# Kernel optimization log

Hardware: AMD Instinct MI355X
Metric: run time of the kernel (lower is better)

Reference implementation:

```python
import jax, jax.numpy as jnp
import numpy as np

B, T, D_IN = 128, 1024, 13
H = 256                      # total CfC units (hidden_units)
N_INTER, N_CMD, N_MOTOR = 77, 51, 128   # AutoNCP(256, 128) layer partition
SIZES = (N_INTER, N_CMD, N_MOTOR)
INS = (D_IN, N_INTER, N_CMD)


def setup_inputs() -> dict:
    key = jax.random.key(0)
    ks = iter(jax.random.split(key, 64))

    def w(shape):
        scale = 1.0 / np.sqrt(shape[-1])
        return jax.random.uniform(next(ks), shape, jnp.float32, -scale, scale)

    inp = {}
    inp["x"] = jax.random.normal(next(ks), (B, T, D_IN), dtype=jnp.float32)
    inp["lstm_Wih"] = w((4 * H, D_IN))
    inp["lstm_Whh"] = w((4 * H, H))
    inp["lstm_bih"] = w((4 * H,))
    inp["lstm_bhh"] = w((4 * H,))
    for l, (nin, nh) in enumerate(zip(INS, SIZES)):
        for nm in ("ff1", "ff2", "ta", "tb"):
            inp[f"l{l}_W{nm}"] = w((nh, nin + nh))
            inp[f"l{l}_b{nm}"] = w((nh,))
        # NCP input sparsity (~0.5 density) + all-ones recurrent block, as WiredCfCCell
        m_in = (jax.random.uniform(next(ks), (nh, nin)) < 0.5).astype(jnp.float32)
        inp[f"l{l}_mask"] = jnp.concatenate([m_in, jnp.ones((nh, nh), jnp.float32)], axis=1)
    inp["gyro_W"] = w((3, N_MOTOR)); inp["gyro_b"] = w((3,))
    inp["acc_W"] = w((3, N_MOTOR)); inp["acc_b"] = w((3,))
    inp["unc_W"] = w((6, N_MOTOR)); inp["unc_b"] = w((6,))
    return inp


def _cfc_cell(z, W1, b1, W2, b2, Wa, ba, Wb, bb, mask):
    # CfC cell, "default" mode, no backbone, ts = 1.0 (CfC called without timespans)
    ff1 = jnp.tanh(z @ (W1 * mask).T + b1)
    ff2 = jnp.tanh(z @ (W2 * mask).T + b2)
    t_interp = jax.nn.sigmoid(z @ Wa.T + ba + z @ Wb.T + bb)  # sigmoid(t_a*1 + t_b)
    return ff1 * (1.0 - t_interp) + t_interp * ff2


def _forward(x, lstm_Wih, lstm_Whh, lstm_bih, lstm_bhh, layer_params, masks,
             gyro_W, gyro_b, acc_W, acc_b, unc_W, unc_b):
    bsz = x.shape[0]
    h0 = jnp.zeros((bsz, H), x.dtype)
    c0 = jnp.zeros((bsz, H), x.dtype)
    b_lstm = lstm_bih + lstm_bhh

    def step(carry, x_t):
        h, c = carry
        # mixed-memory LSTM cell on the full state
        gates = x_t @ lstm_Wih.T + h @ lstm_Whh.T + b_lstm
        i, f, g, o = jnp.split(gates, 4, axis=-1)
        c = jax.nn.sigmoid(f) * c + jax.nn.sigmoid(i) * jnp.tanh(g)
        h = jax.nn.sigmoid(o) * jnp.tanh(c)
        # WiredCfCCell: sequential NCP layers (inter -> command -> motor)
        hs = (h[:, :N_INTER], h[:, N_INTER:N_INTER + N_CMD], h[:, N_INTER + N_CMD:])
        inp = x_t
        new_hs = []
        for l in range(3):
            inp = _cfc_cell(jnp.concatenate([inp, hs[l]], axis=-1), *layer_params[l], masks[l])
            new_hs.append(inp)
        h = jnp.concatenate(new_hs, axis=-1)
        return (h, c), new_hs[-1]

    _, motor = jax.lax.scan(step, (h0, c0), jnp.swapaxes(x, 0, 1))
    motor = jnp.swapaxes(motor, 0, 1)  # (B, T, N_MOTOR)
    pred = jnp.concatenate([motor @ gyro_W.T + gyro_b, motor @ acc_W.T + acc_b], axis=-1)
    uncertainty = jax.nn.softplus(motor @ unc_W.T + unc_b)
    return pred, uncertainty


def reference(x, lstm_Wih, lstm_Whh, lstm_bih, lstm_bhh,
              l0_Wff1, l0_bff1, l0_Wff2, l0_bff2, l0_Wta, l0_bta, l0_Wtb, l0_btb, l0_mask,
              l1_Wff1, l1_bff1, l1_Wff2, l1_bff2, l1_Wta, l1_bta, l1_Wtb, l1_btb, l1_mask,
              l2_Wff1, l2_bff1, l2_Wff2, l2_bff2, l2_Wta, l2_bta, l2_Wtb, l2_btb, l2_mask,
              gyro_W, gyro_b, acc_W, acc_b, unc_W, unc_b):
    layer_params = (
        (l0_Wff1, l0_bff1, l0_Wff2, l0_bff2, l0_Wta, l0_bta, l0_Wtb, l0_btb),
        (l1_Wff1, l1_bff1, l1_Wff2, l1_bff2, l1_Wta, l1_bta, l1_Wtb, l1_btb),
        (l2_Wff1, l2_bff1, l2_Wff2, l2_bff2, l2_Wta, l2_bta, l2_Wtb, l2_btb),
    )
    masks = (l0_mask, l1_mask, l2_mask)
    return _forward(x, lstm_Wih, lstm_Whh, lstm_bih, lstm_bhh, layer_params, masks,
                    gyro_W, gyro_b, acc_W, acc_b, unc_W, unc_b)
```

## Files before the change

kernel.cpp:

```cpp
#include <hip/hip_runtime.h>
#include <cstdint>

#define B_  128
#define T_  1024
#define DIN 13
#define HS  256
#define N0  77
#define N1  51
#define N2  128

#define QG   34
#define NRG  1024
#define Q0   12
#define NR0  308
#define Q1   16
#define NR1  204
#define Q2   23
#define NR2  512
#define Q2LDS 18

#define EXSTRIDE 256
#define X1O   0
#define X2O   128

typedef _Float16 h2_t __attribute__((ext_vector_type(2)));

static __device__ __forceinline__ uint32_t pk2(float a, float b) {
  h2_t v; v.x = (_Float16)a; v.y = (_Float16)b;
  return __builtin_bit_cast(uint32_t, v);
}
static __device__ __forceinline__ unsigned short f16b(float v) {
  return __builtin_bit_cast(unsigned short, (_Float16)v);
}
static __device__ __forceinline__ void st16(void* base, int idx, unsigned short v) {
  ((unsigned short*)base)[idx] = v;
}
static __device__ __forceinline__ float dot2f(uint32_t w, uint32_t z, float acc) {
#if __has_builtin(__builtin_amdgcn_fdot2)
  return __builtin_amdgcn_fdot2(__builtin_bit_cast(h2_t, w), __builtin_bit_cast(h2_t, z), acc, false);
#else
  h2_t a = __builtin_bit_cast(h2_t, w), b = __builtin_bit_cast(h2_t, z);
  return acc + (float)a.x * (float)b.x + (float)a.y * (float)b.y;
#endif
}
static __device__ __forceinline__ float dot8f(uint4 w, uint4 z, float acc) {
  acc = dot2f(w.x, z.x, acc);
  acc = dot2f(w.y, z.y, acc);
  acc = dot2f(w.z, z.z, acc);
  acc = dot2f(w.w, z.w, acc);
  return acc;
}
static __device__ __forceinline__ float sigf(float x) { return 1.f / (1.f + expf(-x)); }

static __device__ __forceinline__ void axpub(int* p, int tag, unsigned short v16) {
  __hip_atomic_store(p, (tag << 16) | (int)v16, __ATOMIC_RELAXED, __HIP_MEMORY_SCOPE_AGENT);
}
static __device__ __forceinline__ unsigned short axpoll(const int* p, int tag) {
  int w;
  do {
    w = __hip_atomic_load((int*)p, __ATOMIC_RELAXED, __HIP_MEMORY_SCOPE_AGENT);
  } while (((unsigned)w >> 16) != (unsigned)tag);
  return (unsigned short)(w & 0xFFFF);
}


__global__ void prep_gates3(const float* __restrict__ Wih, const float* __restrict__ Whh,
                            uint32_t* __restrict__ out) {
  int id = blockIdx.x * blockDim.x + threadIdx.x;
  if (id >= 136 * NRG) return;
  int k2 = id >> 10, row = id & (NRG - 1);
  float v[2];
#pragma unroll
  for (int j = 0; j < 2; ++j) {
    int e = 2 * k2 + j;
    float val = 0.f;
    if (e < 13) val = Wih[row * DIN + e];
    else if (e >= 16 && e < 144) val = Whh[row * HS + 128 + (e - 16)];
    else if (e >= 144 && e < 195) val = Whh[row * HS + 77 + (e - 144)];
    else if (e >= 195 && e < 272) val = Whh[row * HS + (e - 195)];
    v[j] = val;
  }
  out[((k2 >> 2) * NRG + row) * 4 + (k2 & 3)] = pk2(v[0], v[1]);
}

__global__ void prep_cfc2(const float* __restrict__ Wf1, const float* __restrict__ Wf2,
                          const float* __restrict__ Wta, const float* __restrict__ Wtb,
                          const float* __restrict__ mask,
                          int nh, int K, int NR, int K2,
                          int p0n, int p0c, int p1s, int p1n, int p1c,
                          uint32_t* __restrict__ out) {
  int id = blockIdx.x * blockDim.x + threadIdx.x;
  if (id >= NR * K2) return;
  int k2 = id / NR, r = id % NR;
  int mat = r / nh, o = r % nh;
  const float* W = (mat == 0) ? Wf1 : (mat == 1) ? Wf2 : (mat == 2) ? Wta : Wtb;
  float v[2];
#pragma unroll
  for (int j = 0; j < 2; ++j) {
    int e = 2 * k2 + j;
    int col = -1;
    if (e < p0n) col = p0c + e;
    else if (e >= p1s && e < p1s + p1n) col = p1c + (e - p1s);
    float val = 0.f;
    if (col >= 0) {
      val = W[o * K + col];
      if (mat < 2) val *= mask[o * K + col];
    }
    v[j] = val;
  }
  out[((k2 >> 2) * NR + r) * 4 + (k2 & 3)] = pk2(v[0], v[1]);
}


struct SMA {
  uint4 l0w[Q0 * NR0];
  uint4 l1w[Q1 * NR1];
  uint4 zb[2][QG];
  uint4 z0[Q0];
  uint4 z1[Q1];
  float garr[512];
  float ffb[NR0];
  float cb0[NR0];
  float cb1[NR1];
};
struct SMB {
  uint4 l2w[Q2LDS * NR2];
  uint4 zb[2][QG];
  uint4 z2[Q2];
  float garr[512];
  float ffb[NR2];
  float cb2[NR2];
  uint4 hwq[12][16];
  float hb[12];
};
static_assert(sizeof(SMA) <= 163840, "SMA too big");
static_assert(sizeof(SMB) <= 163840, "SMB too big");

struct PArgs {
  const float* x;
  const float* bih; const float* bhh;
  const float* b0[4]; const float* b1[4]; const float* b2[4];
  const float* gW; const float* gb; const float* aW; const float* ab;
  const float* uW; const float* ub;
  const uint4* wsG; const uint4* wsL0; const uint4* wsL1; const uint4* wsL2;
  int* ex;
  float* out;
};

__global__ __launch_bounds__(512, 2) void rnn_coop3(PArgs P) {
  extern __shared__ char smraw[];
  const int tid = threadIdx.x;
  const bool isA = (blockIdx.x < B_);
  const int b = blockIdx.x & (B_ - 1);
  int* EX = P.ex + b * EXSTRIDE;
  const float* xb = P.x + (size_t)b * T_ * DIN;
  const size_t UNC_OFF = (size_t)B_ * T_ * 6;

  if (isA) {
    SMA& sm = *(SMA*)smraw;
    for (int i = tid; i < Q0 * NR0; i += 512) sm.l0w[i] = P.wsL0[i];
    for (int i = tid; i < Q1 * NR1; i += 512) sm.l1w[i] = P.wsL1[i];
    for (int i = tid; i < NR0; i += 512) sm.cb0[i] = P.b0[i / N0][i % N0];
    for (int i = tid; i < NR1; i += 512) sm.cb1[i] = P.b1[i / N1][i % N1];
    {
      uint32_t* zz = (uint32_t*)sm.zb;
      for (int i = tid; i < (2 * QG + Q0 + Q1) * 4; i += 512) zz[i] = 0u;
    }
    const int grow = ((tid >> 7) << 8) | (tid & 127);
    const float bg = P.bih[grow] + P.bhh[grow];
    float c_r = 0.f;
    __syncthreads();
    if (tid < 13) st16(sm.zb[0], tid, f16b(xb[tid]));
    __syncthreads();
    uint4* zbc = sm.zb[0];
    uint4* zbn = sm.zb[1];
    {
      float acc = bg;
      acc = dot8f(P.wsG[0 * NRG + grow], zbc[0], acc);
      acc = dot8f(P.wsG[1 * NRG + grow], zbc[1], acc);
      sm.garr[tid] = acc;
    }
    __syncthreads();

    for (int t = 0; t < T_; ++t) {
      if (tid < 128) {
        float gi = sm.garr[tid], gf = sm.garr[128 + tid];
        float gg = sm.garr[256 + tid], go = sm.garr[384 + tid];
        float cn = sigf(gf) * c_r + sigf(gi) * tanhf(gg);
        c_r = cn;
        float h = sigf(go) * tanhf(cn);
        if (tid < N0) st16(sm.z0, 13 + tid, f16b(h));
        else          st16(sm.z1, tid - N0, f16b(h));
      } else if (tid >= 320 && tid < 336) {
        int i = tid - 320;
        if (i < 13) {
          float xv = (t + 1 < T_) ? xb[(size_t)(t + 1) * DIN + i] : 0.f;
          st16(zbn, i, f16b(xv));
        }
      } else if (tid >= 336 && tid < 352) {
        int i = tid - 336;
        if (i < 13) st16(sm.z0, i, ((unsigned short*)zbc)[i]);
      }
      __syncthreads();
      if (tid < NR0) {
        float a = sm.cb0[tid];
#pragma unroll
        for (int q = 0; q < Q0; ++q) a = dot8f(sm.l0w[q * NR0 + tid], sm.z0[q], a);
        sm.ffb[tid] = (tid < 2 * N0) ? tanhf(a) : a;
      }
      __syncthreads();
      if (tid < N0) {
        float ti = sigf(sm.ffb[2 * N0 + tid] + sm.ffb[3 * N0 + tid]);
        float v = sm.ffb[tid] * (1.f - ti) + ti * sm.ffb[N0 + tid];
        unsigned short v16 = f16b(v);
        axpub(EX + X1O + tid, t + 1, v16);
        st16(sm.z1, 51 + tid, v16);
        st16(zbn, 195 + tid, v16);
      }
      __syncthreads();
      if (tid < NR1) {
        float a = sm.cb1[tid];
#pragma unroll
        for (int q = 0; q < Q1; ++q) a = dot8f(sm.l1w[q * NR1 + tid], sm.z1[q], a);
        sm.ffb[tid] = (tid < 2 * N1) ? tanhf(a) : a;
      }
      __syncthreads();
      if (tid < N1) {
        float ti = sigf(sm.ffb[2 * N1 + tid] + sm.ffb[3 * N1 + tid]);
        float v = sm.ffb[tid] * (1.f - ti) + ti * sm.ffb[N1 + tid];
        unsigned short v16 = f16b(v);
        axpub(EX + X1O + N0 + tid, t + 1, v16);
        st16(zbn, 144 + tid, v16);
      }
      __syncthreads();
      uint4 pw[16];
#pragma unroll
      for (int q = 0; q < 16; ++q) pw[q] = P.wsG[(2 + q) * NRG + grow];
      float acc = bg;
      acc = dot8f(P.wsG[0 * NRG + grow], zbn[0], acc);
      acc = dot8f(P.wsG[1 * NRG + grow], zbn[1], acc);
#pragma unroll 8
      for (int q = 18; q < 34; ++q)
        acc = dot8f(P.wsG[q * NRG + grow], zbn[q], acc);
      asm volatile("" ::: "memory");
      if (tid < 128) {
        unsigned short v16 = axpoll(EX + X2O + tid, t + 1);
        st16(zbn, 16 + tid, v16);
      }
      __syncthreads();
#pragma unroll
      for (int q = 0; q < 16; ++q) acc = dot8f(pw[q], zbn[2 + q], acc);
      sm.garr[tid] = acc;
      __syncthreads();
      uint4* tmp = zbc; zbc = zbn; zbn = tmp;
    }
  } else {
    SMB& sm = *(SMB*)smraw;
    for (int i = tid; i < Q2LDS * NR2; i += 512) sm.l2w[i] = P.wsL2[i];
    for (int i = tid; i < NR2; i += 512) sm.cb2[i] = P.b2[i >> 7][i & 127];
    for (int i = tid; i < 768; i += 512) {
      int r = i >> 6, w = i & 63;
      const float* W = (r < 3) ? P.gW + r * 128 : (r < 6) ? P.aW + (r - 3) * 128 : P.uW + (r - 6) * 128;
      ((uint32_t*)sm.hwq)[i] = pk2(W[2 * w], W[2 * w + 1]);
    }
    if (tid < 12) sm.hb[tid] = (tid < 3) ? P.gb[tid] : (tid < 6) ? P.ab[tid - 3] : P.ub[tid - 6];
    {
      uint32_t* zz = (uint32_t*)sm.zb;
      for (int i = tid; i < (2 * QG + Q2) * 4; i += 512) zz[i] = 0u;
    }
    const int grow = ((tid >> 7) << 8) | 128 | (tid & 127);
    const float bg = P.bih[grow] + P.bhh[grow];
    float c_r = 0.f;
    __syncthreads();
    if (tid < 13) st16(sm.zb[0], tid, f16b(xb[tid]));
    __syncthreads();
    uint4* zbc = sm.zb[0];
    uint4* zbn = sm.zb[1];

    for (int t = 0; t < T_; ++t) {
      float acc = bg;
#pragma unroll 8
      for (int q = 0; q < QG; ++q)
        acc = dot8f(P.wsG[q * NRG + grow], zbc[q], acc);
      if (tid < 12 && t > 0) {
        int r = tid;
        float a = sm.hb[r];
#pragma unroll
        for (int q = 0; q < 16; ++q) a = dot8f(sm.hwq[r][q], zbc[2 + q], a);
        size_t base = ((size_t)b * T_ + (t - 1)) * 6;
        if (r < 6) P.out[base + r] = a;
        else {
          float sp = (a > 0.f) ? (a + log1pf(expf(-a))) : log1pf(expf(a));
          P.out[UNC_OFF + base + (r - 6)] = sp;
        }
      }
      sm.garr[tid] = acc;
      __syncthreads();
      if (tid < 128) {
        float gi = sm.garr[tid], gf = sm.garr[128 + tid];
        float gg = sm.garr[256 + tid], go = sm.garr[384 + tid];
        float cn = sigf(gf) * c_r + sigf(gi) * tanhf(gg);
        c_r = cn;
        float h = sigf(go) * tanhf(cn);
        st16(sm.z2, 56 + tid, f16b(h));
      } else if (tid >= 192 && tid < 208) {
        int i = tid - 192;
        if (i < 13) {
          float xv = (t + 1 < T_) ? xb[(size_t)(t + 1) * DIN + i] : 0.f;
          st16(zbn, i, f16b(xv));
        }
      }
      __syncthreads();
      float a2 = sm.cb2[tid];
#pragma unroll
      for (int q = 7; q < Q2LDS; ++q) a2 = dot8f(sm.l2w[q * NR2 + tid], sm.z2[q], a2);
#pragma unroll
      for (int q = Q2LDS; q < Q2; ++q) a2 = dot8f(P.wsL2[q * NR2 + tid], sm.z2[q], a2);
      if (tid < 128) {
        unsigned short v16 = axpoll(EX + X1O + tid, t + 1);
        if (tid < N0) {
          st16(zbn, 195 + tid, v16);
        } else {
          int j = tid - N0;
          st16(sm.z2, j, v16);
          st16(zbn, 144 + j, v16);
        }
      }
      __syncthreads();
#pragma unroll
      for (int q = 0; q < 7; ++q) a2 = dot8f(sm.l2w[q * NR2 + tid], sm.z2[q], a2);
      sm.ffb[tid] = (tid < 2 * N2) ? tanhf(a2) : a2;
      __syncthreads();
      if (tid < N2) {
        float ti = sigf(sm.ffb[2 * N2 + tid] + sm.ffb[3 * N2 + tid]);
        float v = sm.ffb[tid] * (1.f - ti) + ti * sm.ffb[N2 + tid];
        unsigned short v16 = f16b(v);
        axpub(EX + X2O + tid, t + 1, v16);
        st16(zbn, 16 + tid, v16);
      }
      __syncthreads();
      uint4* tmp = zbc; zbc = zbn; zbn = tmp;
    }
    if (tid < 12) {
      int r = tid;
      float a = sm.hb[r];
#pragma unroll
      for (int q = 0; q < 16; ++q) a = dot8f(sm.hwq[r][q], zbc[2 + q], a);
      size_t base = ((size_t)b * T_ + (T_ - 1)) * 6;
      if (r < 6) P.out[base + r] = a;
      else {
        float sp = (a > 0.f) ? (a + log1pf(expf(-a))) : log1pf(expf(a));
        P.out[UNC_OFF + base + (r - 6)] = sp;
      }
    }
  }
}


struct Args {
  const float* x;
  const float* Wih; const float* Whh; const float* bih; const float* bhh;
  const float* W0[4]; const float* b0[4]; const float* m0;
  const float* W1[4]; const float* b1[4]; const float* m1;
  const float* W2[4]; const float* b2[4]; const float* m2;
  const float* gW; const float* gb; const float* aW; const float* ab;
  const float* uW; const float* ub;
  float* out;
};

struct SMF {
  float xt[16];
  float lstm_h[HS];
  float hprev[HS];
  float garr[4 * HS];
  float ffb[4][128];
  float cb0[NR0];
  float cb1[NR1];
  float cb2[NR2];
  float hw[12][132];
  float hb[12];
};

__global__ __launch_bounds__(512, 2) void rnn_fallback(Args A) {
  extern __shared__ char smraw[];
  SMF& sm = *(SMF*)smraw;
  const int tid = threadIdx.x;
  const int b = blockIdx.x;

  for (int i = tid; i < NR0; i += 512) sm.cb0[i] = A.b0[i / N0][i % N0];
  for (int i = tid; i < NR1; i += 512) sm.cb1[i] = A.b1[i / N1][i % N1];
  for (int i = tid; i < NR2; i += 512) sm.cb2[i] = A.b2[i / N2][i % N2];
  for (int i = tid; i < 12 * 128; i += 512) {
    int r = i >> 7, k = i & 127;
    sm.hw[r][k] = (r < 3) ? A.gW[r * 128 + k]
                : (r < 6) ? A.aW[(r - 3) * 128 + k]
                          : A.uW[(r - 6) * 128 + k];
  }
  if (tid < 12) sm.hb[tid] = (tid < 3) ? A.gb[tid] : (tid < 6) ? A.ab[tid - 3] : A.ub[tid - 6];
  for (int i = tid; i < HS; i += 512) sm.hprev[i] = 0.f;
  float bga = A.bih[tid] + A.bhh[tid];
  float bgb = A.bih[tid + 512] + A.bhh[tid + 512];
  float c_r = 0.f;
  __syncthreads();

  const float* xb = A.x + (size_t)b * T_ * DIN;
  const size_t UNC_OFF = (size_t)B_ * T_ * 6;

  for (int t = 0; t < T_; ++t) {
    const float* xp = xb + (size_t)t * DIN;
    if (tid < DIN) sm.xt[tid] = xp[tid];
    __syncthreads();

    float aa = bga, ab = bgb;
    for (int k = 0; k < DIN; ++k) {
      float xv = sm.xt[k];
      aa += A.Wih[tid * DIN + k] * xv;
      ab += A.Wih[(tid + 512) * DIN + k] * xv;
    }
    for (int k = 0; k < HS; ++k) {
      float hv = sm.hprev[k];
      aa += A.Whh[tid * HS + k] * hv;
      ab += A.Whh[(tid + 512) * HS + k] * hv;
    }
    sm.garr[tid] = aa;
    sm.garr[tid + 512] = ab;
    __syncthreads();

    if (tid < HS) {
      float gi = sm.garr[tid], gf = sm.garr[HS + tid];
      float gg = sm.garr[2 * HS + tid], go = sm.garr[3 * HS + tid];
      float cn = sigf(gf) * c_r + sigf(gi) * tanhf(gg);
      c_r = cn;
      sm.lstm_h[tid] = sigf(go) * tanhf(cn);
    }
    __syncthreads();

    if (tid < NR0) {
      int mat = tid / N0, o = tid % N0;
      const float* W = A.W0[mat];
      const float* m = A.m0;
      const int Kl = DIN + N0;
      float acc = sm.cb0[tid];
      for (int k = 0; k < DIN; ++k) {
        float w = W[o * Kl + k];
        if (mat < 2) w *= m[o * Kl + k];
        acc += w * sm.xt[k];
      }
      for (int k = DIN; k < Kl; ++k) acc += W[o * Kl + k] * sm.lstm_h[k - DIN];
      sm.ffb[mat][o] = (mat < 2) ? tanhf(acc) : acc;
    }
    __syncthreads();
    if (tid < N0) {
      float ti = sigf(sm.ffb[2][tid] + sm.ffb[3][tid]);
      sm.hprev[tid] = sm.ffb[0][tid] * (1.f - ti) + ti * sm.ffb[1][tid];
    }
    __syncthreads();

    if (tid < NR1) {
      int mat = tid / N1, o = tid % N1;
      const float* W = A.W1[mat];
      const float* m = A.m1;
      const int Kl = N0 + N1;
      float acc = sm.cb1[tid];
      for (int k = 0; k < N0; ++k) {
        float w = W[o * Kl + k];
        if (mat < 2) w *= m[o * Kl + k];
        acc += w * sm.hprev[k];
      }
      for (int k = N0; k < Kl; ++k) acc += W[o * Kl + k] * sm.lstm_h[k];
      sm.ffb[mat][o] = (mat < 2) ? tanhf(acc) : acc;
    }
    __syncthreads();
    if (tid < N1) {
      float ti = sigf(sm.ffb[2][tid] + sm.ffb[3][tid]);
      sm.hprev[N0 + tid] = sm.ffb[0][tid] * (1.f - ti) + ti * sm.ffb[1][tid];
    }
    __syncthreads();

    {
      int mat = tid >> 7, o = tid & 127;
      const float* W = A.W2[mat];
      const float* m = A.m2;
      const int Kl = N1 + N2;
      float acc = sm.cb2[tid];
      for (int k = 0; k < N1; ++k) {
        float w = W[o * Kl + k];
        if (mat < 2) w *= m[o * Kl + k];
        acc += w * sm.hprev[N0 + k];
      }
      for (int k = N1; k < Kl; ++k) acc += W[o * Kl + k] * sm.lstm_h[N0 + k];
      sm.ffb[mat][o] = (mat < 2) ? tanhf(acc) : acc;
    }
    __syncthreads();
    if (tid < N2) {
      float ti = sigf(sm.ffb[2][tid] + sm.ffb[3][tid]);
      sm.hprev[N0 + N1 + tid] = sm.ffb[0][tid] * (1.f - ti) + ti * sm.ffb[1][tid];
    }
    __syncthreads();

    if (tid >= 256 && tid < 268) {
      int r = tid - 256;
      const float* mo = &sm.hprev[N0 + N1];
      float acc = sm.hb[r];
      for (int k = 0; k < 128; ++k) acc += sm.hw[r][k] * mo[k];
      size_t base = ((size_t)b * T_ + t) * 6;
      if (r < 6) A.out[base + r] = acc;
      else {
        float sp = (acc > 0.f) ? (acc + log1pf(expf(-acc))) : log1pf(expf(acc));
        A.out[UNC_OFF + base + (r - 6)] = sp;
      }
    }
    __syncthreads();
  }
}


extern "C" void kernel_launch(void* const* d_in, const int* in_sizes, int n_in,
                              void* d_out, int out_size, void* d_ws, size_t ws_size,
                              hipStream_t stream) {
  const float* x   = (const float*)d_in[0];
  const float* Wih = (const float*)d_in[1];
  const float* Whh = (const float*)d_in[2];
  const float* bih = (const float*)d_in[3];
  const float* bhh = (const float*)d_in[4];
  const float *W[3][4], *bb[3][4], *mk[3];
  for (int l = 0; l < 3; ++l) {
    int base = 5 + l * 9;
    for (int nm = 0; nm < 4; ++nm) {
      W[l][nm]  = (const float*)d_in[base + 2 * nm];
      bb[l][nm] = (const float*)d_in[base + 2 * nm + 1];
    }
    mk[l] = (const float*)d_in[base + 8];
  }
  const float* gW = (const float*)d_in[32];
  const float* gb = (const float*)d_in[33];
  const float* aW = (const float*)d_in[34];
  const float* ab = (const float*)d_in[35];
  const float* uW = (const float*)d_in[36];
  const float* ub = (const float*)d_in[37];

  char* ws = (char*)d_ws;
  const size_t szG  = (size_t)QG * NRG * 16;
  const size_t szL0 = (size_t)Q0 * NR0 * 16;
  const size_t szL1 = (size_t)Q1 * NR1 * 16;
  const size_t szL2 = (size_t)Q2 * NR2 * 16;
  const size_t offG = 0, offL0 = szG, offL1 = offL0 + szL0, offL2 = offL1 + szL1;
  const size_t offEx = offL2 + szL2;
  const size_t exBytes = (size_t)B_ * EXSTRIDE * 4;
  const size_t need = offEx + exBytes;

  if (ws_size >= need) {
    PArgs P;
    P.x = x; P.bih = bih; P.bhh = bhh;
    for (int nm = 0; nm < 4; ++nm) { P.b0[nm] = bb[0][nm]; P.b1[nm] = bb[1][nm]; P.b2[nm] = bb[2][nm]; }
    P.gW = gW; P.gb = gb; P.aW = aW; P.ab = ab; P.uW = uW; P.ub = ub;
    P.wsG  = (const uint4*)(ws + offG);
    P.wsL0 = (const uint4*)(ws + offL0);
    P.wsL1 = (const uint4*)(ws + offL1);
    P.wsL2 = (const uint4*)(ws + offL2);
    P.ex   = (int*)(ws + offEx);
    P.out  = (float*)d_out;

    hipMemsetAsync(ws + offEx, 0, exBytes, stream);
    int n;
    n = 136 * NRG;
    prep_gates3<<<(n + 255) / 256, 256, 0, stream>>>(Wih, Whh, (uint32_t*)(ws + offG));
    n = NR0 * 48;
    prep_cfc2<<<(n + 255) / 256, 256, 0, stream>>>(W[0][0], W[0][1], W[0][2], W[0][3], mk[0],
                                                   N0, DIN + N0, NR0, 48,
                                                   90, 0, 96, 0, 0,
                                                   (uint32_t*)(ws + offL0));
    n = NR1 * 64;
    prep_cfc2<<<(n + 255) / 256, 256, 0, stream>>>(W[1][0], W[1][1], W[1][2], W[1][3], mk[1],
                                                   N1, N0 + N1, NR1, 64,
                                                   51, 77, 51, 77, 0,
                                                   (uint32_t*)(ws + offL1));
    n = NR2 * 92;
    prep_cfc2<<<(n + 255) / 256, 256, 0, stream>>>(W[2][0], W[2][1], W[2][2], W[2][3], mk[2],
                                                   N2, N1 + N2, NR2, 92,
                                                   51, 0, 56, 128, 51,
                                                   (uint32_t*)(ws + offL2));
    int lds = (int)((sizeof(SMA) > sizeof(SMB)) ? sizeof(SMA) : sizeof(SMB));
    hipFuncSetAttribute(reinterpret_cast<const void*>(&rnn_coop3),
                        hipFuncAttributeMaxDynamicSharedMemorySize, lds);
    rnn_coop3<<<2 * B_, 512, lds, stream>>>(P);
    return;
  }

  Args A;
  A.x = x; A.Wih = Wih; A.Whh = Whh; A.bih = bih; A.bhh = bhh;
  for (int nm = 0; nm < 4; ++nm) {
    A.W0[nm] = W[0][nm]; A.b0[nm] = bb[0][nm];
    A.W1[nm] = W[1][nm]; A.b1[nm] = bb[1][nm];
    A.W2[nm] = W[2][nm]; A.b2[nm] = bb[2][nm];
  }
  A.m0 = mk[0]; A.m1 = mk[1]; A.m2 = mk[2];
  A.gW = gW; A.gb = gb; A.aW = aW; A.ab = ab; A.uW = uW; A.ub = ub;
  A.out = (float*)d_out;
  hipFuncSetAttribute(reinterpret_cast<const void*>(&rnn_fallback),
                      hipFuncAttributeMaxDynamicSharedMemorySize, (int)sizeof(SMF));
  rnn_fallback<<<B_, 512, sizeof(SMF), stream>>>(A);
}
```

Baseline: 5.430 ms.

## Process two batch elements per block pair to reuse streamed weights

Adds a new kernel in which each producer/consumer block pair handles two batch elements at once. Each weight load from LDS or global memory is reused for two dot products, so the per-step cost of streaming the gate matrix is shared across two sequences. The grid shrinks from 256 to 128 blocks, which cuts parallelism, and register and LDS use per block roughly double. A runtime check on spill (local) memory picks between the new kernel and the old one, and the old kernel's prefetch of the recurrent weights into registers is dropped.

```diff
diff --git a/kernel.cpp b/kernel.cpp
--- a/kernel.cpp
+++ b/kernel.cpp
@@ -19,9 +19,7 @@
 #define NR2  512
 #define Q2LDS 18
 
-#define EXSTRIDE 256
-#define X1O   0
-#define X2O   128
+#define NPAIR 64
 
 typedef _Float16 h2_t __attribute__((ext_vector_type(2)));
 
@@ -111,6 +109,30 @@
   out[((k2 >> 2) * NR + r) * 4 + (k2 & 3)] = pk2(v[0], v[1]);
 }
 
+
+struct SMA2 {
+  uint4 l0w[Q0 * NR0];
+  uint4 l1w[Q1 * NR1];
+  uint4 zb[2][2][QG];
+  uint4 z0[2][Q0];
+  uint4 z1[2][Q1];
+  float garr[2][512];
+  float ffb[2][NR0];
+  float cb0[NR0];
+  float cb1[NR1];
+};
+struct SMB2 {
+  uint4 l2w[Q2LDS * NR2];
+  uint4 zb[2][2][QG];
+  uint4 z2[2][Q2];
+  float garr[2][512];
+  float ffb[2][NR2];
+  float cb2[NR2];
+  uint4 hwq[12][16];
+  float hb[12];
+};
+static_assert(sizeof(SMA2) <= 163840, "SMA2 too big");
+static_assert(sizeof(SMB2) <= 163840, "SMB2 too big");
 
 struct SMA {
   uint4 l0w[Q0 * NR0];
@@ -133,8 +155,6 @@
   uint4 hwq[12][16];
   float hb[12];
 };
-static_assert(sizeof(SMA) <= 163840, "SMA too big");
-static_assert(sizeof(SMB) <= 163840, "SMB too big");
 
 struct PArgs {
   const float* x;
@@ -147,12 +167,282 @@
   float* out;
 };
 
+__global__ __launch_bounds__(512, 2) void rnn_g2(PArgs P) {
+  extern __shared__ char smraw[];
+  const int tid = threadIdx.x;
+  const bool isA = (blockIdx.x < NPAIR);
+  const int pr = blockIdx.x & (NPAIR - 1);
+  int* EX = P.ex + pr * 512;
+  const float* xb0 = P.x + (size_t)(2 * pr) * T_ * DIN;
+  const float* xb1 = xb0 + (size_t)T_ * DIN;
+  const size_t UNC_OFF = (size_t)B_ * T_ * 6;
+
+  if (isA) {
+    SMA2& sm = *(SMA2*)smraw;
+    for (int i = tid; i < Q0 * NR0; i += 512) sm.l0w[i] = P.wsL0[i];
+    for (int i = tid; i < Q1 * NR1; i += 512) sm.l1w[i] = P.wsL1[i];
+    for (int i = tid; i < NR0; i += 512) sm.cb0[i] = P.b0[i / N0][i % N0];
+    for (int i = tid; i < NR1; i += 512) sm.cb1[i] = P.b1[i / N1][i % N1];
+    {
+      uint32_t* zz = (uint32_t*)sm.zb;
+      for (int i = tid; i < (4 * QG + 2 * Q0 + 2 * Q1) * 4; i += 512) zz[i] = 0u;
+    }
+    const int grow = ((tid >> 7) << 8) | (tid & 127);
+    const float bg = P.bih[grow] + P.bhh[grow];
+    float c_r = 0.f;
+    __syncthreads();
+    if (tid < 26) {
+      int e = tid >= 13, i = tid - 13 * e;
+      st16(sm.zb[0][e], i, f16b(e ? xb1[i] : xb0[i]));
+    }
+    __syncthreads();
+    {
+      float a0 = bg, a1 = bg;
+#pragma unroll
+      for (int q = 0; q < 2; ++q) {
+        uint4 w = P.wsG[q * NRG + grow];
+        a0 = dot8f(w, sm.zb[0][0][q], a0);
+        a1 = dot8f(w, sm.zb[0][1][q], a1);
+      }
+      sm.garr[0][tid] = a0;
+      sm.garr[1][tid] = a1;
+    }
+    __syncthreads();
+    int cur = 0;
+
+    for (int t = 0; t < T_; ++t) {
+      const int nxt = cur ^ 1;
+      if (tid < 256) {
+        int e = tid >> 7, u = tid & 127;
+        float gi = sm.garr[e][u], gf = sm.garr[e][128 + u];
+        float gg = sm.garr[e][256 + u], go = sm.garr[e][384 + u];
+        float cn = sigf(gf) * c_r + sigf(gi) * tanhf(gg);
+        c_r = cn;
+        float h = sigf(go) * tanhf(cn);
+        if (u < N0) st16(sm.z0[e], 13 + u, f16b(h));
+        else        st16(sm.z1[e], u - N0, f16b(h));
+      } else if (tid >= 320 && tid < 352) {
+        int j = tid - 320, e = j >> 4, i = j & 15;
+        if (i < 13) {
+          const float* xe = e ? xb1 : xb0;
+          float xv = (t + 1 < T_) ? xe[(size_t)(t + 1) * DIN + i] : 0.f;
+          st16(sm.zb[nxt][e], i, f16b(xv));
+        }
+      } else if (tid >= 352 && tid < 384) {
+        int j = tid - 352, e = j >> 4, i = j & 15;
+        if (i < 13) st16(sm.z0[e], i, ((unsigned short*)sm.zb[cur][e])[i]);
+      }
+      __syncthreads();
+      if (tid < NR0) {
+        float a0 = sm.cb0[tid], a1 = a0;
+#pragma unroll
+        for (int q = 0; q < Q0; ++q) {
+          uint4 w = sm.l0w[q * NR0 + tid];
+          a0 = dot8f(w, sm.z0[0][q], a0);
+          a1 = dot8f(w, sm.z0[1][q], a1);
+        }
+        bool tn = (tid < 2 * N0);
+        sm.ffb[0][tid] = tn ? tanhf(a0) : a0;
+        sm.ffb[1][tid] = tn ? tanhf(a1) : a1;
+      }
+      __syncthreads();
+      if (tid < 2 * N0) {
+        int e = tid >= N0, o = tid - N0 * e;
+        float ti = sigf(sm.ffb[e][2 * N0 + o] + sm.ffb[e][3 * N0 + o]);
+        float v = sm.ffb[e][o] * (1.f - ti) + ti * sm.ffb[e][N0 + o];
+        unsigned short v16 = f16b(v);
+        axpub(EX + e * 256 + o, t + 1, v16);
+        st16(sm.z1[e], 51 + o, v16);
+        st16(sm.zb[nxt][e], 195 + o, v16);
+      }
+      __syncthreads();
+      if (tid < NR1) {
+        float a0 = sm.cb1[tid], a1 = a0;
+#pragma unroll
+        for (int q = 0; q < Q1; ++q) {
+          uint4 w = sm.l1w[q * NR1 + tid];
+          a0 = dot8f(w, sm.z1[0][q], a0);
+          a1 = dot8f(w, sm.z1[1][q], a1);
+        }
+        bool tn = (tid < 2 * N1);
+        sm.ffb[0][tid] = tn ? tanhf(a0) : a0;
+        sm.ffb[1][tid] = tn ? tanhf(a1) : a1;
+      }
+      __syncthreads();
+      if (tid < 2 * N1) {
+        int e = tid >= N1, o = tid - N1 * e;
+        float ti = sigf(sm.ffb[e][2 * N1 + o] + sm.ffb[e][3 * N1 + o]);
+        float v = sm.ffb[e][o] * (1.f - ti) + ti * sm.ffb[e][N1 + o];
+        unsigned short v16 = f16b(v);
+        axpub(EX + e * 256 + N0 + o, t + 1, v16);
+        st16(sm.zb[nxt][e], 144 + o, v16);
+      }
+      __syncthreads();
+      float a0 = bg, a1 = bg;
+#pragma unroll
+      for (int q = 0; q < 2; ++q) {
+        uint4 w = P.wsG[q * NRG + grow];
+        a0 = dot8f(w, sm.zb[nxt][0][q], a0);
+        a1 = dot8f(w, sm.zb[nxt][1][q], a1);
+      }
+#pragma unroll 8
+      for (int q = 18; q < 34; ++q) {
+        uint4 w = P.wsG[q * NRG + grow];
+        a0 = dot8f(w, sm.zb[nxt][0][q], a0);
+        a1 = dot8f(w, sm.zb[nxt][1][q], a1);
+      }
+      if (tid < 256) {
+        int e = tid >> 7, j = tid & 127;
+        unsigned short v16 = axpoll(EX + e * 256 + 128 + j, t + 1);
+        st16(sm.zb[nxt][e], 16 + j, v16);
+      }
+      __syncthreads();
+#pragma unroll 8
+      for (int q = 2; q < 18; ++q) {
+        uint4 w = P.wsG[q * NRG + grow];
+        a0 = dot8f(w, sm.zb[nxt][0][q], a0);
+        a1 = dot8f(w, sm.zb[nxt][1][q], a1);
+      }
+      sm.garr[0][tid] = a0;
+      sm.garr[1][tid] = a1;
+      __syncthreads();
+      cur = nxt;
+    }
+  } else {
+    SMB2& sm = *(SMB2*)smraw;
+    for (int i = tid; i < Q2LDS * NR2; i += 512) sm.l2w[i] = P.wsL2[i];
+    for (int i = tid; i < NR2; i += 512) sm.cb2[i] = P.b2[i >> 7][i & 127];
+    for (int i = tid; i < 768; i += 512) {
+      int r = i >> 6, w = i & 63;
+      const float* W = (r < 3) ? P.gW + r * 128 : (r < 6) ? P.aW + (r - 3) * 128 : P.uW + (r - 6) * 128;
+      ((uint32_t*)sm.hwq)[i] = pk2(W[2 * w], W[2 * w + 1]);
+    }
+    if (tid < 12) sm.hb[tid] = (tid < 3) ? P.gb[tid] : (tid < 6) ? P.ab[tid - 3] : P.ub[tid - 6];
+    {
+      uint32_t* zz = (uint32_t*)sm.zb;
+      for (int i = tid; i < (4 * QG + 2 * Q2) * 4; i += 512) zz[i] = 0u;
+    }
+    const int grow = ((tid >> 7) << 8) | 128 | (tid & 127);
+    const float bg = P.bih[grow] + P.bhh[grow];
+    float c_r = 0.f;
+    __syncthreads();
+    if (tid < 26) {
+      int e = tid >= 13, i = tid - 13 * e;
+      st16(sm.zb[0][e], i, f16b(e ? xb1[i] : xb0[i]));
+    }
+    __syncthreads();
+    int cur = 0;
+
+    for (int t = 0; t < T_; ++t) {
+      const int nxt = cur ^ 1;
+      float a0 = bg, a1 = bg;
+#pragma unroll 8
+      for (int q = 0; q < QG; ++q) {
+        uint4 w = P.wsG[q * NRG + grow];
+        a0 = dot8f(w, sm.zb[cur][0][q], a0);
+        a1 = dot8f(w, sm.zb[cur][1][q], a1);
+      }
+      if (tid < 24 && t > 0) {
+        int e = tid >= 12, r = tid - 12 * e;
+        float a = sm.hb[r];
+#pragma unroll
+        for (int q = 0; q < 16; ++q) a = dot8f(sm.hwq[r][q], sm.zb[cur][e][2 + q], a);
+        size_t base = ((size_t)(2 * pr + e) * T_ + (t - 1)) * 6;
+        if (r < 6) P.out[base + r] = a;
+        else {
+          float sp = (a > 0.f) ? (a + log1pf(expf(-a))) : log1pf(expf(a));
+          P.out[UNC_OFF + base + (r - 6)] = sp;
+        }
+      }
+      sm.garr[0][tid] = a0;
+      sm.garr[1][tid] = a1;
+      __syncthreads();
+      if (tid < 256) {
+        int e = tid >> 7, u = tid & 127;
+        float gi = sm.garr[e][u], gf = sm.garr[e][128 + u];
+        float gg = sm.garr[e][256 + u], go = sm.garr[e][384 + u];
+        float cn = sigf(gf) * c_r + sigf(gi) * tanhf(gg);
+        c_r = cn;
+        float h = sigf(go) * tanhf(cn);
+        st16(sm.z2[e], 56 + u, f16b(h));
+      } else if (tid >= 320 && tid < 352) {
+        int j = tid - 320, e = j >> 4, i = j & 15;
+        if (i < 13) {
+          const float* xe = e ? xb1 : xb0;
+          float xv = (t + 1 < T_) ? xe[(size_t)(t + 1) * DIN + i] : 0.f;
+          st16(sm.zb[nxt][e], i, f16b(xv));
+        }
+      }
+      __syncthreads();
+      float b0a = sm.cb2[tid], b1a = b0a;
+#pragma unroll
+      for (int q = 7; q < Q2LDS; ++q) {
+        uint4 w = sm.l2w[q * NR2 + tid];
+        b0a = dot8f(w, sm.z2[0][q], b0a);
+        b1a = dot8f(w, sm.z2[1][q], b1a);
+      }
+#pragma unroll
+      for (int q = Q2LDS; q < Q2; ++q) {
+        uint4 w = P.wsL2[q * NR2 + tid];
+        b0a = dot8f(w, sm.z2[0][q], b0a);
+        b1a = dot8f(w, sm.z2[1][q], b1a);
+      }
+      if (tid < 256) {
+        int e = tid >> 7, j = tid & 127;
+        unsigned short v16 = axpoll(EX + e * 256 + j, t + 1);
+        if (j < N0) {
+          st16(sm.zb[nxt][e], 195 + j, v16);
+        } else {
+          int o = j - N0;
+          st16(sm.z2[e], o, v16);
+          st16(sm.zb[nxt][e], 144 + o, v16);
+        }
+      }
+      __syncthreads();
+#pragma unroll
+      for (int q = 0; q < 7; ++q) {
+        uint4 w = sm.l2w[q * NR2 + tid];
+        b0a = dot8f(w, sm.z2[0][q], b0a);
+        b1a = dot8f(w, sm.z2[1][q], b1a);
+      }
+      {
+        bool tn = (tid < 2 * N2);
+        sm.ffb[0][tid] = tn ? tanhf(b0a) : b0a;
+        sm.ffb[1][tid] = tn ? tanhf(b1a) : b1a;
+      }
+      __syncthreads();
+      if (tid < 256) {
+        int e = tid >> 7, u = tid & 127;
+        float ti = sigf(sm.ffb[e][2 * N2 + u] + sm.ffb[e][3 * N2 + u]);
+        float v = sm.ffb[e][u] * (1.f - ti) + ti * sm.ffb[e][N2 + u];
+        unsigned short v16 = f16b(v);
+        axpub(EX + e * 256 + 128 + u, t + 1, v16);
+        st16(sm.zb[nxt][e], 16 + u, v16);
+      }
+      __syncthreads();
+      cur = nxt;
+    }
+    if (tid < 24) {
+      int e = tid >= 12, r = tid - 12 * e;
+      float a = sm.hb[r];
+#pragma unroll
+      for (int q = 0; q < 16; ++q) a = dot8f(sm.hwq[r][q], sm.zb[cur][e][2 + q], a);
+      size_t base = ((size_t)(2 * pr + e) * T_ + (T_ - 1)) * 6;
+      if (r < 6) P.out[base + r] = a;
+      else {
+        float sp = (a > 0.f) ? (a + log1pf(expf(-a))) : log1pf(expf(a));
+        P.out[UNC_OFF + base + (r - 6)] = sp;
+      }
+    }
+  }
+}
+
 __global__ __launch_bounds__(512, 2) void rnn_coop3(PArgs P) {
   extern __shared__ char smraw[];
   const int tid = threadIdx.x;
   const bool isA = (blockIdx.x < B_);
   const int b = blockIdx.x & (B_ - 1);
-  int* EX = P.ex + b * EXSTRIDE;
+  int* EX = P.ex + b * 256;
   const float* xb = P.x + (size_t)b * T_ * DIN;
   const size_t UNC_OFF = (size_t)B_ * T_ * 6;
 
@@ -213,7 +503,7 @@
         float ti = sigf(sm.ffb[2 * N0 + tid] + sm.ffb[3 * N0 + tid]);
         float v = sm.ffb[tid] * (1.f - ti) + ti * sm.ffb[N0 + tid];
         unsigned short v16 = f16b(v);
-        axpub(EX + X1O + tid, t + 1, v16);
+        axpub(EX + tid, t + 1, v16);
         st16(sm.z1, 51 + tid, v16);
         st16(zbn, 195 + tid, v16);
       }
@@ -229,27 +519,23 @@
         float ti = sigf(sm.ffb[2 * N1 + tid] + sm.ffb[3 * N1 + tid]);
         float v = sm.ffb[tid] * (1.f - ti) + ti * sm.ffb[N1 + tid];
         unsigned short v16 = f16b(v);
-        axpub(EX + X1O + N0 + tid, t + 1, v16);
+        axpub(EX + N0 + tid, t + 1, v16);
         st16(zbn, 144 + tid, v16);
       }
       __syncthreads();
-      uint4 pw[16];
-#pragma unroll
-      for (int q = 0; q < 16; ++q) pw[q] = P.wsG[(2 + q) * NRG + grow];
       float acc = bg;
       acc = dot8f(P.wsG[0 * NRG + grow], zbn[0], acc);
       acc = dot8f(P.wsG[1 * NRG + grow], zbn[1], acc);
 #pragma unroll 8
       for (int q = 18; q < 34; ++q)
         acc = dot8f(P.wsG[q * NRG + grow], zbn[q], acc);
-      asm volatile("" ::: "memory");
       if (tid < 128) {
-        unsigned short v16 = axpoll(EX + X2O + tid, t + 1);
+        unsigned short v16 = axpoll(EX + 128 + tid, t + 1);
         st16(zbn, 16 + tid, v16);
       }
       __syncthreads();
-#pragma unroll
-      for (int q = 0; q < 16; ++q) acc = dot8f(pw[q], zbn[2 + q], acc);
+#pragma unroll 8
+      for (int q = 2; q < 18; ++q) acc = dot8f(P.wsG[q * NRG + grow], zbn[q], acc);
       sm.garr[tid] = acc;
       __syncthreads();
       uint4* tmp = zbc; zbc = zbn; zbn = tmp;
@@ -317,7 +603,7 @@
 #pragma unroll
       for (int q = Q2LDS; q < Q2; ++q) a2 = dot8f(P.wsL2[q * NR2 + tid], sm.z2[q], a2);
       if (tid < 128) {
-        unsigned short v16 = axpoll(EX + X1O + tid, t + 1);
+        unsigned short v16 = axpoll(EX + tid, t + 1);
         if (tid < N0) {
           st16(zbn, 195 + tid, v16);
         } else {
@@ -335,7 +621,7 @@
         float ti = sigf(sm.ffb[2 * N2 + tid] + sm.ffb[3 * N2 + tid]);
         float v = sm.ffb[tid] * (1.f - ti) + ti * sm.ffb[N2 + tid];
         unsigned short v16 = f16b(v);
-        axpub(EX + X2O + tid, t + 1, v16);
+        axpub(EX + 128 + tid, t + 1, v16);
         st16(zbn, 16 + tid, v16);
       }
       __syncthreads();
@@ -546,7 +832,7 @@
   const size_t szL2 = (size_t)Q2 * NR2 * 16;
   const size_t offG = 0, offL0 = szG, offL1 = offL0 + szL0, offL2 = offL1 + szL1;
   const size_t offEx = offL2 + szL2;
-  const size_t exBytes = (size_t)B_ * EXSTRIDE * 4;
+  const size_t exBytes = 131072;
   const size_t need = offEx + exBytes;
 
   if (ws_size >= need) {
@@ -580,10 +866,23 @@
                                                    N2, N1 + N2, NR2, 92,
                                                    51, 0, 56, 128, 51,
                                                    (uint32_t*)(ws + offL2));
-    int lds = (int)((sizeof(SMA) > sizeof(SMB)) ? sizeof(SMA) : sizeof(SMB));
-    hipFuncSetAttribute(reinterpret_cast<const void*>(&rnn_coop3),
-                        hipFuncAttributeMaxDynamicSharedMemorySize, lds);
-    rnn_coop3<<<2 * B_, 512, lds, stream>>>(P);
+
+    hipFuncAttributes fa{};
+    bool useG2 = false;
+    if (hipFuncGetAttributes(&fa, reinterpret_cast<const void*>(&rnn_g2)) == hipSuccess) {
+      useG2 = (fa.localSizeBytes == 0);
+    }
+    if (useG2) {
+      int lds = (int)sizeof(SMB2);
+      hipFuncSetAttribute(reinterpret_cast<const void*>(&rnn_g2),
+                          hipFuncAttributeMaxDynamicSharedMemorySize, lds);
+      rnn_g2<<<2 * NPAIR, 512, lds, stream>>>(P);
+    } else {
+      int lds = (int)((sizeof(SMA) > sizeof(SMB)) ? sizeof(SMA) : sizeof(SMB));
+      hipFuncSetAttribute(reinterpret_cast<const void*>(&rnn_coop3),
+                          hipFuncAttributeMaxDynamicSharedMemorySize, lds);
+      rnn_coop3<<<2 * B_, 512, lds, stream>>>(P);
+    }
     return;
   }
 
```

Result: faster. 4.816 ms (-11.3%).
